# Kernel optimization log

Hardware: AMD Instinct MI355X
Metric: run time of the kernel (lower is better)

## Reference

```python
import jax, jax.numpy as jnp
import numpy as np

B, N, D, H, DH, DFF = 2, 2048, 1024, 16, 64, 4096
EPS = 1e-5  # F.layer_norm default


def setup_inputs() -> dict:
    key = jax.random.key(0)
    ks = jax.random.split(key, 8)
    w = lambda k, shape: jax.random.normal(k, shape, dtype=jnp.float32) * 0.02
    # standard rotary frequencies over full head dim (rot_dim = DH)
    inv_freq = 1.0 / (10000.0 ** (jnp.arange(0, DH, 2, dtype=jnp.float32) / DH))
    t = jnp.arange(N, dtype=jnp.float32)
    f = t[:, None] * inv_freq[None, :]          # [N, DH/2]
    freqs = jnp.concatenate([f, f], axis=-1)    # [N, DH]
    return {
        "x": jax.random.normal(ks[0], (B, N, D), dtype=jnp.float32),
        "gamma_pre": jnp.ones((D,), jnp.float32),
        "w_qkv": w(ks[1], (3 * D, D)),
        "w_o": w(ks[2], (D, D)),
        "gamma_ff": jnp.ones((D,), jnp.float32),
        "w_up": w(ks[3], (DFF, D)),
        "b_up": jnp.zeros((DFF,), jnp.float32),
        "w_gate": w(ks[4], (DFF, D)),
        "b_gate": jnp.zeros((DFF,), jnp.float32),
        "w_out": w(ks[5], (D, DFF)),
        "b_out": jnp.zeros((D,), jnp.float32),
        "freqs": freqs,
        "mask": jnp.ones((B, N), dtype=bool),
    }


def _layernorm(x, gamma):
    mu = jnp.mean(x, axis=-1, keepdims=True)
    var = jnp.var(x, axis=-1, keepdims=True)
    return (x - mu) * jax.lax.rsqrt(var + EPS) * gamma


def _rotate_half(x):
    x1, x2 = jnp.split(x, 2, axis=-1)
    return jnp.concatenate([-x2, x1], axis=-1)


def _rope(t, freqs):
    # rot_dim == DH so nothing is left unrotated
    return t * jnp.cos(freqs) + _rotate_half(t) * jnp.sin(freqs)


def reference(x, gamma_pre, w_qkv, w_o, gamma_ff, w_up, b_up, w_gate, b_gate,
              w_out, b_out, freqs, mask):
    b, n, d = x.shape
    # ---- self-attention branch (pre-norm) ----
    h = _layernorm(x, gamma_pre)
    qkv = h @ w_qkv.T                                   # [b, n, 3d]
    q, k, v = jnp.split(qkv, 3, axis=-1)
    to_heads = lambda t: t.reshape(b, n, H, DH).transpose(0, 2, 1, 3)  # b h n d
    q, k, v = to_heads(q), to_heads(k), to_heads(v)
    q = _rope(q, freqs)
    k = _rope(k, freqs)
    scale = 1.0 / np.sqrt(DH).astype(np.float32)
    dots = jnp.einsum('bhid,bhjd->bhij', q, k) * scale  # [b, H, n, n]
    neg = -jnp.finfo(dots.dtype).max
    dots = jnp.where(mask[:, None, None, :], dots, neg)        # key padding mask
    causal = jnp.triu(jnp.ones((n, n), dtype=bool), 1)
    dots = jnp.where(causal, neg, dots)
    attn = jax.nn.softmax(dots.astype(jnp.float32), axis=-1).astype(dots.dtype)
    o = jnp.einsum('bhij,bhjd->bhid', attn, v)
    o = o.transpose(0, 2, 1, 3).reshape(b, n, d) @ w_o.T
    o = jnp.where(mask[..., None], o, 0.0)
    x = x + o
    # ---- GLU feed-forward branch (pre-norm) ----
    h2 = _layernorm(x, gamma_ff)
    up = h2 @ w_up.T + b_up
    gate = h2 @ w_gate.T + b_gate
    ff = (up * jax.nn.silu(gate)) @ w_out.T + b_out
    return x + ff
```

## Files before the change

### kernel.cpp

```cpp
#include <hip/hip_runtime.h>
#include <stdint.h>


#define B_ 2
#define N_ 2048
#define D_ 1024
#define H_ 16
#define DFF_ 4096
#define ROWS_ (B_*N_)

typedef unsigned short u16;
typedef short short8 __attribute__((ext_vector_type(8)));
typedef float float4_ __attribute__((ext_vector_type(4)));

#define NEGBIG (-1e30f)
#define QSCALE 0.1803368801111204f

__device__ __forceinline__ float b2f(u16 u) {
  union { unsigned u; float f; } c; c.u = ((unsigned)u) << 16; return c.f;
}
__device__ __forceinline__ u16 f2b(float f) {
  union { float f; unsigned u; } c; c.f = f;
  unsigned x = c.u;
  x += 0x7fffu + ((x >> 16) & 1u);
  return (u16)(x >> 16);
}

__device__ __forceinline__ void gl_lds16(const u16* g, u16* l) {
  __builtin_amdgcn_global_load_lds(
      (const __attribute__((address_space(1))) unsigned int*)g,
      (__attribute__((address_space(3))) unsigned int*)l, 16, 0, 0);
}

__global__ __launch_bounds__(256) void cvt_kernel(const float* __restrict__ src,
                                                  u16* __restrict__ dst, int n) {
  int i = (blockIdx.x * 256 + threadIdx.x) * 8;
  if (i >= n) return;
  float4_ v0 = *(const float4_*)(src + i);
  float4_ v1 = *(const float4_*)(src + i + 4);
  short8 pk;
#pragma unroll
  for (int e = 0; e < 4; e++) { pk[e] = (short)f2b(v0[e]); pk[4 + e] = (short)f2b(v1[e]); }
  *(short8*)(dst + i) = pk;
}

__global__ __launch_bounds__(256) void ln_kernel(const float* __restrict__ xin,
                                                 const float* __restrict__ gamma,
                                                 u16* __restrict__ out) {
  int row = blockIdx.x, t = threadIdx.x;
  float4_ v = *(const float4_*)(xin + (size_t)row * D_ + t * 4);
  float s = 0.f, ss = 0.f;
#pragma unroll
  for (int i = 0; i < 4; i++) { s += v[i]; ss += v[i] * v[i]; }
#pragma unroll
  for (int off = 1; off < 64; off <<= 1) {
    s  += __shfl_xor(s, off, 64);
    ss += __shfl_xor(ss, off, 64);
  }
  __shared__ float red[8];
  if ((t & 63) == 0) { red[t >> 6] = s; red[4 + (t >> 6)] = ss; }
  __syncthreads();
  s  = red[0] + red[1] + red[2] + red[3];
  ss = red[4] + red[5] + red[6] + red[7];
  float mu  = s * (1.f / D_);
  float var = ss * (1.f / D_) - mu * mu;
  float rs  = rsqrtf(var + 1e-5f);
#pragma unroll
  for (int i = 0; i < 4; i++)
    out[(size_t)row * D_ + t * 4 + i] = f2b((v[i] - mu) * rs * gamma[t * 4 + i]);
}

template <int MODE>
__device__ __forceinline__ void gemm_epilogue(float4_ (&acc)[4][4], void* Cout,
                                              const float* bias, const void* extra,
                                              int mbase, int nbase, int N,
                                              int wr, int wc, int quad, int l16) {
#pragma unroll
  for (int i = 0; i < 4; i++) {
#pragma unroll
    for (int r = 0; r < 4; r++) {
      int row = mbase + wr * 64 + i * 16 + quad * 4 + r;
#pragma unroll
      for (int j = 0; j < 4; j++) {
        int col = nbase + wc * 64 + j * 16 + l16;
        size_t idx = (size_t)row * N + col;
        float v = acc[i][j][r];
        if (MODE == 0) {
          ((u16*)Cout)[idx] = f2b(v);
        } else if (MODE == 1) {
          ((u16*)Cout)[idx] = f2b(v + bias[col]);
        } else if (MODE == 2) {
          ((float*)Cout)[idx] = v + ((const float*)extra)[idx];
        } else if (MODE == 3) {
          float gate = v + bias[col];
          float sig = 1.f / (1.f + expf(-gate));
          float upv = b2f(((const u16*)extra)[idx]);
          ((u16*)Cout)[idx] = f2b(upv * gate * sig);
        } else {
          ((float*)Cout)[idx] = v + bias[col] + ((const float*)extra)[idx];
        }
      }
    }
  }
}

__device__ __forceinline__ void gemm_core(const u16* A, const u16* W,
                                          float4_ (&acc)[4][4], u16* sA, u16* sW,
                                          int mbase, int nbase, int K,
                                          int klo, int khi,
                                          int wave, int lane, int wr, int wc,
                                          int quad, int l16) {
  for (int k0 = klo; k0 < khi; k0 += 32) {
    __syncthreads();
#pragma unroll
    for (int it = 0; it < 2; it++) {
      int c = wave * 128 + it * 64 + lane;
      int row = c >> 2, col = (c & 3) << 3;
      gl_lds16(A + (size_t)(mbase + row) * K + k0 + col, sA + (size_t)(wave * 128 + it * 64) * 8);
      gl_lds16(W + (size_t)(nbase + row) * K + k0 + col, sW + (size_t)(wave * 128 + it * 64) * 8);
    }
    __syncthreads();
    short8 af[4], bf[4];
#pragma unroll
    for (int i = 0; i < 4; i++)
      af[i] = *(const short8*)(sA + (wr * 64 + i * 16 + l16) * 32 + quad * 8);
#pragma unroll
    for (int j = 0; j < 4; j++)
      bf[j] = *(const short8*)(sW + (wc * 64 + j * 16 + l16) * 32 + quad * 8);
#pragma unroll
    for (int i = 0; i < 4; i++)
#pragma unroll
      for (int j = 0; j < 4; j++)
        acc[i][j] = __builtin_amdgcn_mfma_f32_16x16x32_bf16(af[i], bf[j], acc[i][j], 0, 0, 0);
  }
}

template <int MODE>
__global__ __launch_bounds__(256) void gemm_bb(const u16* __restrict__ A,
                                               const u16* __restrict__ W,
                                               void* Cout,
                                               const float* __restrict__ bias,
                                               const void* extra,
                                               int M, int N, int K) {
  __shared__ __align__(16) u16 sA[128 * 32];
  __shared__ __align__(16) u16 sW[128 * 32];
  int t = threadIdx.x;
  int mbase = blockIdx.y * 128, nbase = blockIdx.x * 128;
  int wave = t >> 6, lane = t & 63;
  int wr = wave >> 1, wc = wave & 1;
  int quad = lane >> 4, l16 = lane & 15;

  float4_ z4 = {0.f, 0.f, 0.f, 0.f};
  float4_ acc[4][4];
#pragma unroll
  for (int i = 0; i < 4; i++)
#pragma unroll
    for (int j = 0; j < 4; j++) acc[i][j] = z4;

  gemm_core(A, W, acc, sA, sW, mbase, nbase, K, 0, K, wave, lane, wr, wc, quad, l16);
  gemm_epilogue<MODE>(acc, Cout, bias, extra, mbase, nbase, N, wr, wc, quad, l16);
}

__global__ __launch_bounds__(256) void gemm_glu2(const u16* __restrict__ A,
                                                 const u16* __restrict__ Wu,
                                                 const u16* __restrict__ Wg,
                                                 const float* __restrict__ bu,
                                                 const float* __restrict__ bg,
                                                 u16* __restrict__ G,
                                                 int M, int N, int K) {
  __shared__ __align__(16) u16 smem[8192];
  u16* sA = smem;
  u16* sU = smem + 4096;
  u16* sG = smem + 6144;
  int t = threadIdx.x;
  int mbase = blockIdx.y * 128, nbase = blockIdx.x * 64;
  int wave = t >> 6, lane = t & 63;
  int mhalf = wave & 1, gsel = wave >> 1;
  int quad = lane >> 4, l16 = lane & 15;

  float4_ z4 = {0.f, 0.f, 0.f, 0.f};
  float4_ acc[4][4];
#pragma unroll
  for (int i = 0; i < 4; i++)
#pragma unroll
    for (int j = 0; j < 4; j++) acc[i][j] = z4;

  for (int k0 = 0; k0 < K; k0 += 32) {
    __syncthreads();
#pragma unroll
    for (int it = 0; it < 2; it++) {
      int c = it * 256 + wave * 64 + lane;
      int row = c >> 2, col = (c & 3) << 3;
      gl_lds16(A + (size_t)(mbase + row) * K + k0 + col, sA + (size_t)(it * 256 + wave * 64) * 8);
    }
    {
      int c = wave * 64 + lane;
      int row = c >> 2, col = (c & 3) << 3;
      size_t go = (size_t)(nbase + row) * K + k0 + col;
      gl_lds16(Wu + go, sU + (size_t)(wave * 64) * 8);
      gl_lds16(Wg + go, sG + (size_t)(wave * 64) * 8);
    }
    __syncthreads();
    short8 af[4], bf[4];
    const u16* sW = gsel ? sG : sU;
#pragma unroll
    for (int i = 0; i < 4; i++)
      af[i] = *(const short8*)(sA + (mhalf * 64 + i * 16 + l16) * 32 + quad * 8);
#pragma unroll
    for (int j = 0; j < 4; j++)
      bf[j] = *(const short8*)(sW + (j * 16 + l16) * 32 + quad * 8);
#pragma unroll
    for (int i = 0; i < 4; i++)
#pragma unroll
      for (int j = 0; j < 4; j++)
        acc[i][j] = __builtin_amdgcn_mfma_f32_16x16x32_bf16(af[i], bf[j], acc[i][j], 0, 0, 0);
  }

  __syncthreads();
  u16* ex = smem + mhalf * 4096;
  if (gsel) {
#pragma unroll
    for (int i = 0; i < 4; i++)
#pragma unroll
      for (int r = 0; r < 4; r++)
#pragma unroll
        for (int j = 0; j < 4; j++) {
          int col = nbase + j * 16 + l16;
          float gv = acc[i][j][r] + bg[col];
          float sig = 1.f / (1.f + expf(-gv));
          ex[(i * 16 + quad * 4 + r) * 64 + j * 16 + l16] = f2b(gv * sig);
        }
  }
  __syncthreads();
  if (!gsel) {
#pragma unroll
    for (int i = 0; i < 4; i++)
#pragma unroll
      for (int r = 0; r < 4; r++) {
        int row = mbase + mhalf * 64 + i * 16 + quad * 4 + r;
#pragma unroll
        for (int j = 0; j < 4; j++) {
          int col = nbase + j * 16 + l16;
          float uv = acc[i][j][r] + bu[col];
          float sg = b2f(ex[(i * 16 + quad * 4 + r) * 64 + j * 16 + l16]);
          G[(size_t)row * N + col] = f2b(uv * sg);
        }
      }
  }
}

__global__ __launch_bounds__(256) void gemm_bb_split(const u16* __restrict__ A,
                                                     const u16* __restrict__ W,
                                                     u16* __restrict__ p0,
                                                     u16* __restrict__ p1,
                                                     int M, int N, int K) {
  __shared__ __align__(16) u16 sA[128 * 32];
  __shared__ __align__(16) u16 sW[128 * 32];
  int t = threadIdx.x;
  int mbase = blockIdx.y * 128, nbase = blockIdx.x * 128;
  int z = blockIdx.z;
  int wave = t >> 6, lane = t & 63;
  int wr = wave >> 1, wc = wave & 1;
  int quad = lane >> 4, l16 = lane & 15;
  int Kh = K >> 1;

  float4_ z4 = {0.f, 0.f, 0.f, 0.f};
  float4_ acc[4][4];
#pragma unroll
  for (int i = 0; i < 4; i++)
#pragma unroll
    for (int j = 0; j < 4; j++) acc[i][j] = z4;

  gemm_core(A, W, acc, sA, sW, mbase, nbase, K, z * Kh, z * Kh + Kh,
            wave, lane, wr, wc, quad, l16);

  u16* P = z ? p1 : p0;
#pragma unroll
  for (int i = 0; i < 4; i++)
#pragma unroll
    for (int r = 0; r < 4; r++) {
      int row = mbase + wr * 64 + i * 16 + quad * 4 + r;
#pragma unroll
      for (int j = 0; j < 4; j++) {
        int col = nbase + wc * 64 + j * 16 + l16;
        P[(size_t)row * N + col] = f2b(acc[i][j][r]);
      }
    }
}

__global__ __launch_bounds__(256) void split_combine(const u16* __restrict__ p0,
                                                     const u16* __restrict__ p1,
                                                     const float* __restrict__ bias,
                                                     const float* __restrict__ resid,
                                                     float* __restrict__ out, int N) {
  int idx = (blockIdx.x * 256 + threadIdx.x) * 8;
  int col = idx & (N - 1);
  short8 a = *(const short8*)(p0 + idx);
  short8 b = *(const short8*)(p1 + idx);
  float4_ r0 = *(const float4_*)(resid + idx);
  float4_ r1 = *(const float4_*)(resid + idx + 4);
  float4_ o0, o1;
#pragma unroll
  for (int e = 0; e < 4; e++) {
    float bb0 = bias ? bias[col + e] : 0.f;
    float bb1 = bias ? bias[col + 4 + e] : 0.f;
    o0[e] = b2f((u16)a[e]) + b2f((u16)b[e]) + bb0 + r0[e];
    o1[e] = b2f((u16)a[4 + e]) + b2f((u16)b[4 + e]) + bb1 + r1[e];
  }
  *(float4_*)(out + idx) = o0;
  *(float4_*)(out + idx + 4) = o1;
}

template <int MODE>
__global__ __launch_bounds__(256) void gemm_nt(const u16* __restrict__ A,
                                               const float* __restrict__ W,
                                               void* Cout,
                                               const float* __restrict__ bias,
                                               const void* extra,
                                               int M, int N, int K) {
  __shared__ __align__(16) u16 sA[128 * 32];
  __shared__ __align__(16) u16 sW[128 * 32];
  int t = threadIdx.x;
  int mbase = blockIdx.y * 128, nbase = blockIdx.x * 128;
  int wave = t >> 6, lane = t & 63;
  int wr = wave >> 1, wc = wave & 1;
  int quad = lane >> 4, l16 = lane & 15;

  float4_ z4 = {0.f, 0.f, 0.f, 0.f};
  float4_ acc[4][4];
#pragma unroll
  for (int i = 0; i < 4; i++)
#pragma unroll
    for (int j = 0; j < 4; j++) acc[i][j] = z4;

  for (int k0 = 0; k0 < K; k0 += 32) {
    __syncthreads();
#pragma unroll
    for (int it = 0; it < 2; it++) {
      int c = t + 256 * it;
      int row = c >> 2, col = (c & 3) << 3;
      ((short8*)sA)[c] = *(const short8*)(A + (size_t)(mbase + row) * K + k0 + col);
      const float* wp = W + (size_t)(nbase + row) * K + k0 + col;
      float4_ w0 = *(const float4_*)wp;
      float4_ w1 = *(const float4_*)(wp + 4);
      short8 pk;
#pragma unroll
      for (int e = 0; e < 4; e++) { pk[e] = (short)f2b(w0[e]); pk[4 + e] = (short)f2b(w1[e]); }
      ((short8*)sW)[c] = pk;
    }
    __syncthreads();
    short8 af[4], bf[4];
#pragma unroll
    for (int i = 0; i < 4; i++)
      af[i] = *(const short8*)(sA + (wr * 64 + i * 16 + l16) * 32 + quad * 8);
#pragma unroll
    for (int j = 0; j < 4; j++)
      bf[j] = *(const short8*)(sW + (wc * 64 + j * 16 + l16) * 32 + quad * 8);
#pragma unroll
    for (int i = 0; i < 4; i++)
#pragma unroll
      for (int j = 0; j < 4; j++)
        acc[i][j] = __builtin_amdgcn_mfma_f32_16x16x32_bf16(af[i], bf[j], acc[i][j], 0, 0, 0);
  }
  gemm_epilogue<MODE>(acc, Cout, bias, extra, mbase, nbase, N, wr, wc, quad, l16);
}

__global__ __launch_bounds__(256) void rope_kernel(const u16* __restrict__ qkv,
                                                   const float* __restrict__ freqs,
                                                   u16* __restrict__ qr,
                                                   u16* __restrict__ kr,
                                                   u16* __restrict__ vt) {
  int idx = blockIdx.x * 256 + threadIdx.x;
  int d2 = idx & 31;
  int h  = (idx >> 5) & 15;
  int n  = (idx >> 9) & 2047;
  int b  = idx >> 20;
  float f = freqs[n * 64 + d2];
  float c = cosf(f), s = sinf(f);
  size_t base = (size_t)(b * N_ + n) * 3072;
  int hd = h * 64 + d2;
  float q1 = b2f(qkv[base + hd]),        q2 = b2f(qkv[base + hd + 32]);
  float k1 = b2f(qkv[base + 1024 + hd]), k2 = b2f(qkv[base + 1024 + hd + 32]);
  float v1 = b2f(qkv[base + 2048 + hd]), v2 = b2f(qkv[base + 2048 + hd + 32]);
  size_t ro = ((size_t)(b * H_ + h) * N_ + n) * 64 + d2;
  qr[ro]      = f2b((q1 * c - q2 * s) * QSCALE);
  qr[ro + 32] = f2b((q2 * c + q1 * s) * QSCALE);
  kr[ro]      = f2b(k1 * c - k2 * s);
  kr[ro + 32] = f2b(k2 * c + k1 * s);
  size_t vo = ((size_t)(b * H_ + h) * 64 + d2) * N_ + n;
  vt[vo]           = f2b(v1);
  vt[vo + 32 * N_] = f2b(v2);
}

#define LP 72
__global__ __launch_bounds__(256) void attn_kernel(const u16* __restrict__ qr,
                                                   const u16* __restrict__ kr,
                                                   const u16* __restrict__ vt,
                                                   u16* __restrict__ opart,
                                                   float* __restrict__ mlp) {
  __shared__ __align__(16) u16 sK[64 * LP];
  __shared__ __align__(16) u16 sV[64 * LP];
  __shared__ __align__(16) u16 sP[4][16 * LP];
  int qp = blockIdx.x, bh = blockIdx.y, sp = blockIdx.z;
  int t = threadIdx.x, wave = t >> 6, lane = t & 63;
  int quad = lane >> 4, l16 = lane & 15;
  const u16* qptr = qr + (size_t)bh * N_ * 64;
  const u16* kp = kr + (size_t)bh * N_ * 64;
  const u16* vp = vt + (size_t)bh * 64 * N_;
  float4_ z4 = {0.f, 0.f, 0.f, 0.f};

  for (int qsel = 0; qsel < 2; qsel++) {
    int qt = qsel ? (N_ / 64 - 1 - qp) : qp;
    int qbase = qt * 64;
    int ntiles = qt + 1, half = (ntiles + 1) >> 1;
    int ktlo = sp ? half : 0, kthi = sp ? ntiles : half;

    short8 aq[2];
    int qrow = qbase + wave * 16 + l16;
#pragma unroll
    for (int kk = 0; kk < 2; kk++)
      aq[kk] = *(const short8*)(qptr + (size_t)qrow * 64 + kk * 32 + quad * 8);

    float4_ o[4] = {z4, z4, z4, z4};
    float m_r[4] = {NEGBIG, NEGBIG, NEGBIG, NEGBIG};
    float l_r[4] = {0.f, 0.f, 0.f, 0.f};

    for (int kt = ktlo; kt < kthi; kt++) {
      __syncthreads();
      {
        const u16* src = kp + (size_t)kt * 64 * 64;
#pragma unroll
        for (int it = 0; it < 2; it++) {
          int c = t + 256 * it;
          int row = c >> 3, seg = c & 7;
          *(short8*)(sK + row * LP + seg * 8) = *(const short8*)(src + c * 8);
          *(short8*)(sV + row * LP + seg * 8) =
              *(const short8*)(vp + (size_t)row * N_ + kt * 64 + seg * 8);
        }
      }
      __syncthreads();

      float4_ sf[4];
#pragma unroll
      for (int j = 0; j < 4; j++) {
        short8 bk0 = *(const short8*)(sK + (j * 16 + l16) * LP + quad * 8);
        short8 bk1 = *(const short8*)(sK + (j * 16 + l16) * LP + 32 + quad * 8);
        float4_ acc = z4;
        acc = __builtin_amdgcn_mfma_f32_16x16x32_bf16(aq[0], bk0, acc, 0, 0, 0);
        acc = __builtin_amdgcn_mfma_f32_16x16x32_bf16(aq[1], bk1, acc, 0, 0, 0);
        sf[j] = acc;
      }
      if (kt == qt) {
#pragma unroll
        for (int j = 0; j < 4; j++)
#pragma unroll
          for (int r = 0; r < 4; r++) {
            int ig = qbase + wave * 16 + quad * 4 + r;
            int jg = kt * 64 + j * 16 + l16;
            if (jg > ig) sf[j][r] = NEGBIG;
          }
      }

#pragma unroll
      for (int r = 0; r < 4; r++) {
        float mt = fmaxf(fmaxf(sf[0][r], sf[1][r]), fmaxf(sf[2][r], sf[3][r]));
#pragma unroll
        for (int off = 1; off < 16; off <<= 1) mt = fmaxf(mt, __shfl_xor(mt, off, 64));
        float mn = fmaxf(m_r[r], mt);
        float alpha = exp2f(m_r[r] - mn);
        float rowsum = 0.f;
#pragma unroll
        for (int j = 0; j < 4; j++) {
          float p = exp2f(sf[j][r] - mn);
          sf[j][r] = p;
          rowsum += p;
        }
#pragma unroll
        for (int off = 1; off < 16; off <<= 1) rowsum += __shfl_xor(rowsum, off, 64);
        l_r[r] = l_r[r] * alpha + rowsum;
        m_r[r] = mn;
#pragma unroll
        for (int jo = 0; jo < 4; jo++) o[jo][r] *= alpha;
      }

      u16* sPw = sP[wave];
#pragma unroll
      for (int j = 0; j < 4; j++)
#pragma unroll
        for (int r = 0; r < 4; r++)
          sPw[(quad * 4 + r) * LP + j * 16 + l16] = f2b(sf[j][r]);
      short8 ap[2];
#pragma unroll
      for (int kk = 0; kk < 2; kk++)
        ap[kk] = *(const short8*)(sPw + l16 * LP + kk * 32 + quad * 8);
#pragma unroll
      for (int jo = 0; jo < 4; jo++)
#pragma unroll
        for (int kk = 0; kk < 2; kk++) {
          short8 bv = *(const short8*)(sV + (jo * 16 + l16) * LP + kk * 32 + quad * 8);
          o[jo] = __builtin_amdgcn_mfma_f32_16x16x32_bf16(ap[kk], bv, o[jo], 0, 0, 0);
        }
    }

#pragma unroll
    for (int r = 0; r < 4; r++) {
      int n = qbase + wave * 16 + quad * 4 + r;
      size_t row = (size_t)bh * N_ + n;
      if (l16 == 0) {
        mlp[2 * (sp * (size_t)65536 + row)]     = m_r[r];
        mlp[2 * (sp * (size_t)65536 + row) + 1] = l_r[r];
      }
#pragma unroll
      for (int jo = 0; jo < 4; jo++)
        opart[sp * (size_t)4194304 + row * 64 + jo * 16 + l16] = f2b(o[jo][r]);
    }
  }
}

__global__ __launch_bounds__(256) void attn_combine(const u16* __restrict__ opart,
                                                    const float* __restrict__ mlp,
                                                    u16* __restrict__ obuf) {
  int idx = blockIdx.x * 256 + threadIdx.x;
  int row = idx >> 3, seg = idx & 7;
  float m0 = mlp[2 * row],                 l0 = mlp[2 * row + 1];
  float m1 = mlp[2 * (65536 + row)],       l1 = mlp[2 * (65536 + row) + 1];
  float mmax = fmaxf(m0, m1);
  float w0 = exp2f(m0 - mmax), w1 = exp2f(m1 - mmax);
  float inv = 1.f / (l0 * w0 + l1 * w1);
  short8 a = *(const short8*)(opart + (size_t)row * 64 + seg * 8);
  short8 b = *(const short8*)(opart + (size_t)4194304 + (size_t)row * 64 + seg * 8);
  short8 r;
#pragma unroll
  for (int e = 0; e < 8; e++)
    r[e] = (short)f2b((b2f((u16)a[e]) * w0 + b2f((u16)b[e]) * w1) * inv);
  int bh = row >> 11, n = row & 2047;
  int bb = bh >> 4, h = bh & 15;
  *(short8*)(obuf + ((size_t)(bb * N_ + n) * D_) + h * 64 + seg * 8) = r;
}

extern "C" void kernel_launch(void* const* d_in, const int* in_sizes, int n_in,
                              void* d_out, int out_size, void* d_ws, size_t ws_size,
                              hipStream_t stream) {
  const float* x         = (const float*)d_in[0];
  const float* gamma_pre = (const float*)d_in[1];
  const float* w_qkv     = (const float*)d_in[2];
  const float* w_o       = (const float*)d_in[3];
  const float* gamma_ff  = (const float*)d_in[4];
  const float* w_up      = (const float*)d_in[5];
  const float* b_up      = (const float*)d_in[6];
  const float* w_gate    = (const float*)d_in[7];
  const float* b_gate    = (const float*)d_in[8];
  const float* w_out     = (const float*)d_in[9];
  const float* b_out     = (const float*)d_in[10];
  const float* freqs     = (const float*)d_in[11];

  char* ws = (char*)d_ws;
  const size_t MB = 1024 * 1024;
  u16*  h     = (u16*)(ws);
  u16*  qkv   = (u16*)(ws + 8 * MB);
  u16*  qr    = (u16*)(ws + 32 * MB);
  u16*  kr    = (u16*)(ws + 40 * MB);
  u16*  vtb   = (u16*)(ws + 48 * MB);
  u16*  ob    = (u16*)(ws + 56 * MB);
  u16*  opart = (u16*)(ws);
  float* mlb  = (float*)(ws + 16 * MB);
  float* x1   = (float*)(ws + 8 * MB);
  u16*  h2    = (u16*)(ws + 24 * MB);
  u16*  g     = (u16*)(ws + 32 * MB);
  u16*  sp0   = (u16*)(ws);
  u16*  sp1   = (u16*)(ws + 24 * MB);
  float* out  = (float*)d_out;

  bool wide = ws_size >= 96 * MB;
  u16* wb_qkv  = (u16*)(ws + 64 * MB);
  u16* wb_o    = (u16*)(ws + 70 * MB);
  u16* wb_up   = (u16*)(ws + 72 * MB);
  u16* wb_gate = (u16*)(ws + 80 * MB);
  u16* wb_out  = (u16*)(ws + 88 * MB);

  if (wide) {
    cvt_kernel<<<(3 * D_ * D_) / 2048, 256, 0, stream>>>(w_qkv, wb_qkv, 3 * D_ * D_);
    cvt_kernel<<<(D_ * D_) / 2048, 256, 0, stream>>>(w_o, wb_o, D_ * D_);
    cvt_kernel<<<(DFF_ * D_) / 2048, 256, 0, stream>>>(w_up, wb_up, DFF_ * D_);
    cvt_kernel<<<(DFF_ * D_) / 2048, 256, 0, stream>>>(w_gate, wb_gate, DFF_ * D_);
    cvt_kernel<<<(DFF_ * D_) / 2048, 256, 0, stream>>>(w_out, wb_out, D_ * DFF_);
  }

  ln_kernel<<<ROWS_, 256, 0, stream>>>(x, gamma_pre, h);
  if (wide)
    gemm_bb<0><<<dim3(3072 / 128, ROWS_ / 128), 256, 0, stream>>>(
        h, wb_qkv, qkv, nullptr, nullptr, ROWS_, 3072, 1024);
  else
    gemm_nt<0><<<dim3(3072 / 128, ROWS_ / 128), 256, 0, stream>>>(
        h, w_qkv, qkv, nullptr, nullptr, ROWS_, 3072, 1024);
  rope_kernel<<<(B_ * N_ * H_ * 32) / 256, 256, 0, stream>>>(qkv, freqs, qr, kr, vtb);
  attn_kernel<<<dim3(N_ / 128, B_ * H_, 2), 256, 0, stream>>>(qr, kr, vtb, opart, mlb);
  attn_combine<<<(B_ * H_ * N_ * 8) / 256, 256, 0, stream>>>(opart, mlb, ob);
  if (wide) {
    gemm_bb_split<<<dim3(1024 / 128, ROWS_ / 128, 2), 256, 0, stream>>>(
        ob, wb_o, sp0, sp1, ROWS_, 1024, 1024);
    split_combine<<<(ROWS_ * 1024) / 2048, 256, 0, stream>>>(
        sp0, sp1, nullptr, x, x1, 1024);
    ln_kernel<<<ROWS_, 256, 0, stream>>>(x1, gamma_ff, h2);
    gemm_glu2<<<dim3(4096 / 64, ROWS_ / 128), 256, 0, stream>>>(
        h2, wb_up, wb_gate, b_up, b_gate, g, ROWS_, 4096, 1024);
    gemm_bb_split<<<dim3(1024 / 128, ROWS_ / 128, 2), 256, 0, stream>>>(
        g, wb_out, sp0, sp1, ROWS_, 1024, 4096);
    split_combine<<<(ROWS_ * 1024) / 2048, 256, 0, stream>>>(
        sp0, sp1, b_out, x1, out, 1024);
  } else {
    gemm_nt<2><<<dim3(1024 / 128, ROWS_ / 128), 256, 0, stream>>>(
        ob, w_o, x1, nullptr, x, ROWS_, 1024, 1024);
    ln_kernel<<<ROWS_, 256, 0, stream>>>(x1, gamma_ff, h2);
    gemm_nt<1><<<dim3(4096 / 128, ROWS_ / 128), 256, 0, stream>>>(
        h2, w_up, g, b_up, nullptr, ROWS_, 4096, 1024);
    gemm_nt<3><<<dim3(4096 / 128, ROWS_ / 128), 256, 0, stream>>>(
        h2, w_gate, g, b_gate, g, ROWS_, 4096, 1024);
    gemm_nt<4><<<dim3(1024 / 128, ROWS_ / 128), 256, 0, stream>>>(
        g, w_out, (void*)out, b_out, x1, ROWS_, 1024, 4096);
  }
}
```

Before: 516.8 us.

## Merge weight conversions, split-K the QKV GEMM, fuse residual combine with LayerNorm

Replaces the five weight-conversion launches with a single kernel that picks its source tensor by block index. The QKV projection becomes a split-K GEMM whose two bf16 partials are summed inside the RoPE kernel. The residual add after the output projection is fused with the second LayerNorm. Buffers are remapped, and the output buffer serves as scratch for K and V. The aim is fewer launches and round trips through memory, and more blocks in flight for the QKV GEMM. In exchange the QKV partials are stored in bf16, which costs some precision.

Result: faster. 505.8 us (-2.1%).

```diff
diff --git a/kernel.cpp b/kernel.cpp
--- a/kernel.cpp
+++ b/kernel.cpp
@@ -10,6 +10,7 @@
 #define ROWS_ (B_*N_)
 
 typedef unsigned short u16;
+typedef short short4_ __attribute__((ext_vector_type(4)));
 typedef short short8 __attribute__((ext_vector_type(8)));
 typedef float float4_ __attribute__((ext_vector_type(4)));
 
@@ -32,10 +33,24 @@
       (__attribute__((address_space(3))) unsigned int*)l, 16, 0, 0);
 }
 
-__global__ __launch_bounds__(256) void cvt_kernel(const float* __restrict__ src,
-                                                  u16* __restrict__ dst, int n) {
-  int i = (blockIdx.x * 256 + threadIdx.x) * 8;
-  if (i >= n) return;
+__global__ __launch_bounds__(256) void cvt_all(const float* __restrict__ s_qkv,
+                                               const float* __restrict__ s_o,
+                                               const float* __restrict__ s_up,
+                                               const float* __restrict__ s_gate,
+                                               const float* __restrict__ s_out,
+                                               u16* __restrict__ d_qkv,
+                                               u16* __restrict__ d_o,
+                                               u16* __restrict__ d_up,
+                                               u16* __restrict__ d_gate,
+                                               u16* __restrict__ d_out_) {
+  int c = blockIdx.x * 256 + threadIdx.x;
+  const float* src; u16* dst; int off;
+  if (c < 393216)       { src = s_qkv;  dst = d_qkv;  off = c; }
+  else if (c < 524288)  { src = s_o;    dst = d_o;    off = c - 393216; }
+  else if (c < 1048576) { src = s_up;   dst = d_up;   off = c - 524288; }
+  else if (c < 1572864) { src = s_gate; dst = d_gate; off = c - 1048576; }
+  else                  { src = s_out;  dst = d_out_; off = c - 1572864; }
+  int i = off * 8;
   float4_ v0 = *(const float4_*)(src + i);
   float4_ v1 = *(const float4_*)(src + i + 4);
   short8 pk;
@@ -68,6 +83,43 @@
 #pragma unroll
   for (int i = 0; i < 4; i++)
     out[(size_t)row * D_ + t * 4 + i] = f2b((v[i] - mu) * rs * gamma[t * 4 + i]);
+}
+
+__global__ __launch_bounds__(256) void combine_ln(const u16* __restrict__ p0,
+                                                  const u16* __restrict__ p1,
+                                                  const float* __restrict__ resid,
+                                                  const float* __restrict__ gamma,
+                                                  float* __restrict__ x1,
+                                                  u16* __restrict__ h2out) {
+  int row = blockIdx.x, t = threadIdx.x;
+  size_t base = (size_t)row * D_ + t * 4;
+  short4_ a = *(const short4_*)(p0 + base);
+  short4_ b = *(const short4_*)(p1 + base);
+  float4_ rv = *(const float4_*)(resid + base);
+  float4_ v;
+  float s = 0.f, ss = 0.f;
+#pragma unroll
+  for (int i = 0; i < 4; i++) {
+    v[i] = b2f((u16)a[i]) + b2f((u16)b[i]) + rv[i];
+    s += v[i]; ss += v[i] * v[i];
+  }
+  *(float4_*)(x1 + base) = v;
+#pragma unroll
+  for (int off = 1; off < 64; off <<= 1) {
+    s  += __shfl_xor(s, off, 64);
+    ss += __shfl_xor(ss, off, 64);
+  }
+  __shared__ float red[8];
+  if ((t & 63) == 0) { red[t >> 6] = s; red[4 + (t >> 6)] = ss; }
+  __syncthreads();
+  s  = red[0] + red[1] + red[2] + red[3];
+  ss = red[4] + red[5] + red[6] + red[7];
+  float mu  = s * (1.f / D_);
+  float var = ss * (1.f / D_) - mu * mu;
+  float rs  = rsqrtf(var + 1e-5f);
+#pragma unroll
+  for (int i = 0; i < 4; i++)
+    h2out[base + i] = f2b((v[i] - mu) * rs * gamma[t * 4 + i]);
 }
 
 template <int MODE>
@@ -135,32 +187,6 @@
   }
 }
 
-template <int MODE>
-__global__ __launch_bounds__(256) void gemm_bb(const u16* __restrict__ A,
-                                               const u16* __restrict__ W,
-                                               void* Cout,
-                                               const float* __restrict__ bias,
-                                               const void* extra,
-                                               int M, int N, int K) {
-  __shared__ __align__(16) u16 sA[128 * 32];
-  __shared__ __align__(16) u16 sW[128 * 32];
-  int t = threadIdx.x;
-  int mbase = blockIdx.y * 128, nbase = blockIdx.x * 128;
-  int wave = t >> 6, lane = t & 63;
-  int wr = wave >> 1, wc = wave & 1;
-  int quad = lane >> 4, l16 = lane & 15;
-
-  float4_ z4 = {0.f, 0.f, 0.f, 0.f};
-  float4_ acc[4][4];
-#pragma unroll
-  for (int i = 0; i < 4; i++)
-#pragma unroll
-    for (int j = 0; j < 4; j++) acc[i][j] = z4;
-
-  gemm_core(A, W, acc, sA, sW, mbase, nbase, K, 0, K, wave, lane, wr, wc, quad, l16);
-  gemm_epilogue<MODE>(acc, Cout, bias, extra, mbase, nbase, N, wr, wc, quad, l16);
-}
-
 __global__ __launch_bounds__(256) void gemm_glu2(const u16* __restrict__ A,
                                                  const u16* __restrict__ Wu,
                                                  const u16* __restrict__ Wg,
@@ -365,7 +391,9 @@
   gemm_epilogue<MODE>(acc, Cout, bias, extra, mbase, nbase, N, wr, wc, quad, l16);
 }
 
-__global__ __launch_bounds__(256) void rope_kernel(const u16* __restrict__ qkv,
+template <int SPLIT>
+__global__ __launch_bounds__(256) void rope_kernel(const u16* __restrict__ q0,
+                                                   const u16* __restrict__ q1,
                                                    const float* __restrict__ freqs,
                                                    u16* __restrict__ qr,
                                                    u16* __restrict__ kr,
@@ -379,17 +407,19 @@
   float c = cosf(f), s = sinf(f);
   size_t base = (size_t)(b * N_ + n) * 3072;
   int hd = h * 64 + d2;
-  float q1 = b2f(qkv[base + hd]),        q2 = b2f(qkv[base + hd + 32]);
-  float k1 = b2f(qkv[base + 1024 + hd]), k2 = b2f(qkv[base + 1024 + hd + 32]);
-  float v1 = b2f(qkv[base + 2048 + hd]), v2 = b2f(qkv[base + 2048 + hd + 32]);
+#define LD(o) (SPLIT ? (b2f(q0[base + (o)]) + b2f(q1[base + (o)])) : b2f(q0[base + (o)]))
+  float v_q1 = LD(hd),        v_q2 = LD(hd + 32);
+  float v_k1 = LD(1024 + hd), v_k2 = LD(1024 + hd + 32);
+  float v_v1 = LD(2048 + hd), v_v2 = LD(2048 + hd + 32);
+#undef LD
   size_t ro = ((size_t)(b * H_ + h) * N_ + n) * 64 + d2;
-  qr[ro]      = f2b((q1 * c - q2 * s) * QSCALE);
-  qr[ro + 32] = f2b((q2 * c + q1 * s) * QSCALE);
-  kr[ro]      = f2b(k1 * c - k2 * s);
-  kr[ro + 32] = f2b(k2 * c + k1 * s);
+  qr[ro]      = f2b((v_q1 * c - v_q2 * s) * QSCALE);
+  qr[ro + 32] = f2b((v_q2 * c + v_q1 * s) * QSCALE);
+  kr[ro]      = f2b(v_k1 * c - v_k2 * s);
+  kr[ro + 32] = f2b(v_k2 * c + v_k1 * s);
   size_t vo = ((size_t)(b * H_ + h) * 64 + d2) * N_ + n;
-  vt[vo]           = f2b(v1);
-  vt[vo + 32 * N_] = f2b(v2);
+  vt[vo]           = f2b(v_v1);
+  vt[vo + 32 * N_] = f2b(v_v2);
 }
 
 #define LP 72
@@ -556,59 +586,69 @@
 
   char* ws = (char*)d_ws;
   const size_t MB = 1024 * 1024;
-  u16*  h     = (u16*)(ws);
-  u16*  qkv   = (u16*)(ws + 8 * MB);
-  u16*  qr    = (u16*)(ws + 32 * MB);
-  u16*  kr    = (u16*)(ws + 40 * MB);
-  u16*  vtb   = (u16*)(ws + 48 * MB);
-  u16*  ob    = (u16*)(ws + 56 * MB);
-  u16*  opart = (u16*)(ws);
-  float* mlb  = (float*)(ws + 16 * MB);
-  float* x1   = (float*)(ws + 8 * MB);
-  u16*  h2    = (u16*)(ws + 24 * MB);
-  u16*  g     = (u16*)(ws + 32 * MB);
-  u16*  sp0   = (u16*)(ws);
-  u16*  sp1   = (u16*)(ws + 24 * MB);
-  float* out  = (float*)d_out;
-
+  float* out = (float*)d_out;
   bool wide = ws_size >= 96 * MB;
-  u16* wb_qkv  = (u16*)(ws + 64 * MB);
-  u16* wb_o    = (u16*)(ws + 70 * MB);
-  u16* wb_up   = (u16*)(ws + 72 * MB);
-  u16* wb_gate = (u16*)(ws + 80 * MB);
-  u16* wb_out  = (u16*)(ws + 88 * MB);
 
   if (wide) {
-    cvt_kernel<<<(3 * D_ * D_) / 2048, 256, 0, stream>>>(w_qkv, wb_qkv, 3 * D_ * D_);
-    cvt_kernel<<<(D_ * D_) / 2048, 256, 0, stream>>>(w_o, wb_o, D_ * D_);
-    cvt_kernel<<<(DFF_ * D_) / 2048, 256, 0, stream>>>(w_up, wb_up, DFF_ * D_);
-    cvt_kernel<<<(DFF_ * D_) / 2048, 256, 0, stream>>>(w_gate, wb_gate, DFF_ * D_);
-    cvt_kernel<<<(DFF_ * D_) / 2048, 256, 0, stream>>>(w_out, wb_out, D_ * DFF_);
-  }
-
-  ln_kernel<<<ROWS_, 256, 0, stream>>>(x, gamma_pre, h);
-  if (wide)
-    gemm_bb<0><<<dim3(3072 / 128, ROWS_ / 128), 256, 0, stream>>>(
-        h, wb_qkv, qkv, nullptr, nullptr, ROWS_, 3072, 1024);
-  else
-    gemm_nt<0><<<dim3(3072 / 128, ROWS_ / 128), 256, 0, stream>>>(
-        h, w_qkv, qkv, nullptr, nullptr, ROWS_, 3072, 1024);
-  rope_kernel<<<(B_ * N_ * H_ * 32) / 256, 256, 0, stream>>>(qkv, freqs, qr, kr, vtb);
-  attn_kernel<<<dim3(N_ / 128, B_ * H_, 2), 256, 0, stream>>>(qr, kr, vtb, opart, mlb);
-  attn_combine<<<(B_ * H_ * N_ * 8) / 256, 256, 0, stream>>>(opart, mlb, ob);
-  if (wide) {
+    u16*  h     = (u16*)(ws);
+    u16*  qp0   = (u16*)(ws + 32 * MB);
+    u16*  qp1   = (u16*)(ws + 8 * MB);
+    u16*  qr    = (u16*)(ws + 56 * MB);
+    u16*  kr    = (u16*)d_out;
+    u16*  vtb   = (u16*)d_out + 4194304;
+    u16*  opart = (u16*)(ws);
+    float* mlb  = (float*)(ws + 16 * MB);
+    u16*  ob    = (u16*)(ws + 24 * MB);
+    u16*  sp0   = (u16*)(ws);
+    u16*  sp1o  = (u16*)(ws + 32 * MB);
+    float* x1   = (float*)(ws + 8 * MB);
+    u16*  h2    = (u16*)(ws + 24 * MB);
+    u16*  g     = (u16*)(ws + 32 * MB);
+    u16*  sp1f  = (u16*)(ws + 24 * MB);
+    u16* wb_qkv  = (u16*)(ws + 64 * MB);
+    u16* wb_o    = (u16*)(ws + 70 * MB);
+    u16* wb_up   = (u16*)(ws + 72 * MB);
+    u16* wb_gate = (u16*)(ws + 80 * MB);
+    u16* wb_out  = (u16*)(ws + 88 * MB);
+
+    cvt_all<<<8192, 256, 0, stream>>>(w_qkv, w_o, w_up, w_gate, w_out,
+                                      wb_qkv, wb_o, wb_up, wb_gate, wb_out);
+    ln_kernel<<<ROWS_, 256, 0, stream>>>(x, gamma_pre, h);
+    gemm_bb_split<<<dim3(3072 / 128, ROWS_ / 128, 2), 256, 0, stream>>>(
+        h, wb_qkv, qp0, qp1, ROWS_, 3072, 1024);
+    rope_kernel<1><<<(B_ * N_ * H_ * 32) / 256, 256, 0, stream>>>(
+        qp0, qp1, freqs, qr, kr, vtb);
+    attn_kernel<<<dim3(N_ / 128, B_ * H_, 2), 256, 0, stream>>>(qr, kr, vtb, opart, mlb);
+    attn_combine<<<(B_ * H_ * N_ * 8) / 256, 256, 0, stream>>>(opart, mlb, ob);
     gemm_bb_split<<<dim3(1024 / 128, ROWS_ / 128, 2), 256, 0, stream>>>(
-        ob, wb_o, sp0, sp1, ROWS_, 1024, 1024);
-    split_combine<<<(ROWS_ * 1024) / 2048, 256, 0, stream>>>(
-        sp0, sp1, nullptr, x, x1, 1024);
-    ln_kernel<<<ROWS_, 256, 0, stream>>>(x1, gamma_ff, h2);
+        ob, wb_o, sp0, sp1o, ROWS_, 1024, 1024);
+    combine_ln<<<ROWS_, 256, 0, stream>>>(sp0, sp1o, x, gamma_ff, x1, h2);
     gemm_glu2<<<dim3(4096 / 64, ROWS_ / 128), 256, 0, stream>>>(
         h2, wb_up, wb_gate, b_up, b_gate, g, ROWS_, 4096, 1024);
     gemm_bb_split<<<dim3(1024 / 128, ROWS_ / 128, 2), 256, 0, stream>>>(
-        g, wb_out, sp0, sp1, ROWS_, 1024, 4096);
+        g, wb_out, sp0, sp1f, ROWS_, 1024, 4096);
     split_combine<<<(ROWS_ * 1024) / 2048, 256, 0, stream>>>(
-        sp0, sp1, b_out, x1, out, 1024);
+        sp0, sp1f, b_out, x1, out, 1024);
   } else {
+    u16*  h     = (u16*)(ws);
+    u16*  qkv   = (u16*)(ws + 8 * MB);
+    u16*  qr    = (u16*)(ws + 32 * MB);
+    u16*  kr    = (u16*)(ws + 40 * MB);
+    u16*  vtb   = (u16*)(ws + 48 * MB);
+    u16*  ob    = (u16*)(ws + 56 * MB);
+    u16*  opart = (u16*)(ws);
+    float* mlb  = (float*)(ws + 16 * MB);
+    float* x1   = (float*)(ws + 8 * MB);
+    u16*  h2    = (u16*)(ws + 24 * MB);
+    u16*  g     = (u16*)(ws + 32 * MB);
+
+    ln_kernel<<<ROWS_, 256, 0, stream>>>(x, gamma_pre, h);
+    gemm_nt<0><<<dim3(3072 / 128, ROWS_ / 128), 256, 0, stream>>>(
+        h, w_qkv, qkv, nullptr, nullptr, ROWS_, 3072, 1024);
+    rope_kernel<0><<<(B_ * N_ * H_ * 32) / 256, 256, 0, stream>>>(
+        qkv, qkv, freqs, qr, kr, vtb);
+    attn_kernel<<<dim3(N_ / 128, B_ * H_, 2), 256, 0, stream>>>(qr, kr, vtb, opart, mlb);
+    attn_combine<<<(B_ * H_ * N_ * 8) / 256, 256, 0, stream>>>(opart, mlb, ob);
     gemm_nt<2><<<dim3(1024 / 128, ROWS_ / 128), 256, 0, stream>>>(
         ob, w_o, x1, nullptr, x, ROWS_, 1024, 1024);
     ln_kernel<<<ROWS_, 256, 0, stream>>>(x1, gamma_ff, h2);
```
